# Optimization experiments

Hardware: AMD Instinct MI355X
Metric: run time of the kernel (lower is better)

The kernel has to match this reference:

```python
import jax, jax.numpy as jnp
import numpy as np

INPUT_SIZE = 512
HIDDEN_SIZE = 512
BATCH = 64
SEQ_LEN = 512


def _xavier(key, shape):
    fan_in, fan_out = shape[0], shape[1]
    limit = float(np.sqrt(6.0 / (fan_in + fan_out)))
    return jax.random.uniform(key, shape, jnp.float32, -limit, limit)


def setup_inputs() -> dict:
    key = jax.random.key(0)
    ks = jax.random.split(key, 14)
    inp = {
        "inputs": jax.random.normal(ks[0], (BATCH, SEQ_LEN, INPUT_SIZE), jnp.float32),
        "W_i": _xavier(ks[1], (INPUT_SIZE, HIDDEN_SIZE)),
        "W_f": _xavier(ks[2], (INPUT_SIZE, HIDDEN_SIZE)),
        "W_o": _xavier(ks[3], (INPUT_SIZE, HIDDEN_SIZE)),
        "W_c": _xavier(ks[4], (INPUT_SIZE, HIDDEN_SIZE)),
        "U_i": _xavier(ks[5], (HIDDEN_SIZE, HIDDEN_SIZE)),
        "U_f": _xavier(ks[6], (HIDDEN_SIZE, HIDDEN_SIZE)),
        "U_o": _xavier(ks[7], (HIDDEN_SIZE, HIDDEN_SIZE)),
        "U_c": _xavier(ks[8], (HIDDEN_SIZE, HIDDEN_SIZE)),
        "b_i": _xavier(ks[9], (1, HIDDEN_SIZE)),
        "b_f": _xavier(ks[10], (1, HIDDEN_SIZE)),
        "b_o": _xavier(ks[11], (1, HIDDEN_SIZE)),
        "b_c": _xavier(ks[12], (1, HIDDEN_SIZE)),
    }
    return inp


def reference(inputs, W_i, W_f, W_o, W_c, U_i, U_f, U_o, U_c, b_i, b_f, b_o, b_c):
    B, S, D = inputs.shape
    H = W_i.shape[1]
    # Fuse the 4 input projections into one GEMM over the whole sequence
    # (same math as per-step separate matmuls, just batched).
    W = jnp.concatenate([W_i, W_f, W_o, W_c], axis=1)      # [D, 4H]
    U = jnp.concatenate([U_i, U_f, U_o, U_c], axis=1)      # [H, 4H]
    b = jnp.concatenate([b_i, b_f, b_o, b_c], axis=1)      # [1, 4H]
    x_proj = jnp.einsum('bsd,dg->sbg', inputs, W) + b      # [S, B, 4H]

    def step(carry, xp):
        h, c = carry
        gates = xp + h @ U                                  # [B, 4H]
        i_g = jax.nn.sigmoid(gates[:, 0*H:1*H])
        f_g = jax.nn.sigmoid(gates[:, 1*H:2*H])
        o_g = jax.nn.sigmoid(gates[:, 2*H:3*H])
        c_t = jnp.tanh(gates[:, 3*H:4*H])
        c_new = f_g * c + i_g * c_t
        h_new = o_g * jnp.tanh(c_new)
        return (h_new, c_new), None

    h0 = jnp.zeros((B, H), jnp.float32)
    c0 = jnp.zeros((B, H), jnp.float32)
    (h_final, _), _ = jax.lax.scan(step, (h0, c0), x_proj)
    return h_final
```

## Files before the change

### kernel.cpp

```cpp
#include <hip/hip_runtime.h>


#define NGROUP 4
#define NSLICE 32
#define GROWS  16
#define SCOLS  16
#define DIM    512
#define HID    512
#define SEQ    512
#define NTHR   256
#define NWG    (NGROUP*NSLICE)

#define AOFF 0
#define BOFF 16384
#define LDS_BYTES (BOFF + 64*2048)

#define WS_CNT_BYTES 1024
#define HBUF_ELEMS   (2*NGROUP*GROWS*HID)
#define WS_NEED      (WS_CNT_BYTES + HBUF_ELEMS*2)

typedef float f32x4  __attribute__((ext_vector_type(4)));
typedef short bf16x8 __attribute__((ext_vector_type(8)));

__device__ __forceinline__ unsigned short f2bf(float f){
  union { float f; unsigned u; } v; v.f = f;
  unsigned r = v.u + 0x7fffu + ((v.u >> 16) & 1u);
  return (unsigned short)(r >> 16);
}
__device__ __forceinline__ float sigm(float x){ return 1.0f/(1.0f + __expf(-x)); }
__device__ __forceinline__ float tanh_f(float x){
  float e = __expf(-2.0f * fabsf(x));
  float t = (1.0f - e)/(1.0f + e);
  return x < 0.0f ? -t : t;
}

__global__ void zero_ws_kernel(uint4* p, int n4){
  int i = blockIdx.x*blockDim.x + threadIdx.x;
  uint4 z; z.x=0u; z.y=0u; z.z=0u; z.w=0u;
  if (i < n4) p[i] = z;
}

__global__ __launch_bounds__(NTHR, 1) void lstm_persistent(
  const float* __restrict__ x,
  const float* __restrict__ W0, const float* __restrict__ W1,
  const float* __restrict__ W2, const float* __restrict__ W3,
  const float* __restrict__ U0, const float* __restrict__ U1,
  const float* __restrict__ U2, const float* __restrict__ U3,
  const float* __restrict__ b0, const float* __restrict__ b1,
  const float* __restrict__ b2, const float* __restrict__ b3,
  float* __restrict__ out,
  unsigned* __restrict__ cnt,
  unsigned short* __restrict__ hbuf)
{
  __shared__ __align__(16) char smem[LDS_BYTES];
  const int tid = threadIdx.x;
  const int bid = blockIdx.x;
  const int g = bid >> 5;
  const int s = bid & 31;
  const int w = tid >> 6;
  const int l = tid & 63;

  {
    const int c    = tid & 63;
    const int kq   = tid >> 6;
    const int gate = c >> 4;
    const int cc   = c & 15;
    const int col  = s*SCOLS + cc;
    const float* Wsrc = (gate==0)?W0:(gate==1)?W1:(gate==2)?W2:W3;
    const float* Usrc = (gate==0)?U0:(gate==1)?U1:(gate==2)?U2:U3;
    const unsigned swz = (unsigned)((c & 7) << 4);
    char* Bp = &smem[BOFF + c*2048];
    #pragma unroll 4
    for (int k = kq*256; k < kq*256 + 256; ++k){
      float v = (k < DIM) ? Wsrc[(size_t)k*HID + col]
                          : Usrc[(size_t)(k-DIM)*HID + col];
      *(unsigned short*)(Bp + (((unsigned)(k*2)) ^ swz)) = f2bf(v);
    }
  }

  const int er = tid >> 4;
  const int ec = tid & 15;
  const int ecol = s*SCOLS + ec;
  const float bi = b0[ecol], bff = b1[ecol], bo = b2[ecol], bc = b3[ecol];
  float cstate = 0.0f;
  float hout   = 0.0f;

  const int arow = l & 15;
  const int qh   = l >> 4;
  const unsigned swzA = (unsigned)((arow & 7) << 4);
  const int bcol = w*16 + arow;
  const unsigned swzB = (unsigned)((bcol & 7) << 4);
  const char* Abase = &smem[AOFF + arow*1024];
  const char* Bbase = &smem[BOFF + bcol*2048];
  float* gatesLds = (float*)&smem[AOFF];

  const int sr  = tid >> 4;
  const int sdb = tid & 15;
  const unsigned swzS = (unsigned)((sr & 7) << 4);
  char* Arow = &smem[AOFF + sr*1024];

  unsigned* mycnt = &cnt[g*32];

  __syncthreads();

#define GEMM_STEP(QA, QB, ACC) do { \
    bf16x8 a_ = *(const bf16x8*)(Abase + (((unsigned)((QA)*64 + qh*16)) ^ swzA)); \
    bf16x8 b_ = *(const bf16x8*)(Bbase + (((unsigned)((QB)*64 + qh*16)) ^ swzB)); \
    ACC = __builtin_amdgcn_mfma_f32_16x16x32_bf16(a_, b_, ACC, 0, 0, 0); \
  } while(0)

  for (int t = 0; t < SEQ; ++t){
    {
      const float* xp = x + ((size_t)(g*GROWS + sr)*SEQ + (size_t)t)*DIM + sdb*32;
      #pragma unroll
      for (int j = 0; j < 4; ++j){
        f32x4 u = *(const f32x4*)(xp + j*8);
        f32x4 v = *(const f32x4*)(xp + j*8 + 4);
        bf16x8 o8;
        o8[0]=(short)f2bf(u[0]); o8[1]=(short)f2bf(u[1]);
        o8[2]=(short)f2bf(u[2]); o8[3]=(short)f2bf(u[3]);
        o8[4]=(short)f2bf(v[0]); o8[5]=(short)f2bf(v[1]);
        o8[6]=(short)f2bf(v[2]); o8[7]=(short)f2bf(v[3]);
        *(bf16x8*)(Arow + (((unsigned)(sdb*64 + j*16)) ^ swzS)) = o8;
      }
    }
    __syncthreads();

    f32x4 acc0 = {0.f,0.f,0.f,0.f}, acc1 = {0.f,0.f,0.f,0.f};
    f32x4 acc2 = {0.f,0.f,0.f,0.f}, acc3 = {0.f,0.f,0.f,0.f};

    #pragma unroll
    for (int q4 = 0; q4 < 4; ++q4){
      GEMM_STEP(q4*4+0, q4*4+0, acc0);
      GEMM_STEP(q4*4+1, q4*4+1, acc1);
      GEMM_STEP(q4*4+2, q4*4+2, acc2);
      GEMM_STEP(q4*4+3, q4*4+3, acc3);
    }

    if (t > 0 && tid == 0){
      const unsigned target = (unsigned)(32*t);
      while (__hip_atomic_load(mycnt, __ATOMIC_ACQUIRE, __HIP_MEMORY_SCOPE_AGENT) < target)
        __builtin_amdgcn_s_sleep(1);
    }
    __syncthreads();

    {
      const unsigned short* hsrc =
        hbuf + ((size_t)((t&1)*NGROUP + g)*GROWS + sr)*HID + sdb*32;
      #pragma unroll
      for (int j = 0; j < 4; ++j){
        bf16x8 hv = *(const bf16x8*)(hsrc + j*8);
        *(bf16x8*)(Arow + (((unsigned)(sdb*64 + j*16)) ^ swzS)) = hv;
      }
    }
    __syncthreads();

    #pragma unroll
    for (int q4 = 0; q4 < 4; ++q4){
      GEMM_STEP(q4*4+0, q4*4+16, acc0);
      GEMM_STEP(q4*4+1, q4*4+17, acc1);
      GEMM_STEP(q4*4+2, q4*4+18, acc2);
      GEMM_STEP(q4*4+3, q4*4+19, acc3);
    }
    __syncthreads();

    f32x4 accs = (acc0 + acc1) + (acc2 + acc3);
    #pragma unroll
    for (int rr = 0; rr < 4; ++rr)
      gatesLds[(qh*4 + rr)*64 + w*16 + arow] = accs[rr];
    __syncthreads();

    {
      float gi = gatesLds[er*64 +  0 + ec] + bi;
      float gf = gatesLds[er*64 + 16 + ec] + bff;
      float go = gatesLds[er*64 + 32 + ec] + bo;
      float gc = gatesLds[er*64 + 48 + ec] + bc;
      float ig = sigm(gi), fg = sigm(gf), og = sigm(go), ct = tanh_f(gc);
      cstate = fg*cstate + ig*ct;
      hout = og * tanh_f(cstate);
      hbuf[((size_t)(((t+1)&1)*NGROUP + g)*GROWS + er)*HID + s*SCOLS + ec] = f2bf(hout);
    }
    __syncthreads();

    if (tid == 0)
      __hip_atomic_fetch_add(mycnt, 1u, __ATOMIC_RELEASE, __HIP_MEMORY_SCOPE_AGENT);
  }

  out[(size_t)(g*GROWS + er)*HID + s*SCOLS + ec] = hout;
#undef GEMM_STEP
}

extern "C" void kernel_launch(void* const* d_in, const int* in_sizes, int n_in,
                              void* d_out, int out_size, void* d_ws, size_t ws_size,
                              hipStream_t stream)
{
  (void)in_sizes; (void)n_in; (void)out_size;
  if (ws_size < (size_t)WS_NEED) return;

  const float* x  = (const float*)d_in[0];
  const float* W0 = (const float*)d_in[1];
  const float* W1 = (const float*)d_in[2];
  const float* W2 = (const float*)d_in[3];
  const float* W3 = (const float*)d_in[4];
  const float* U0 = (const float*)d_in[5];
  const float* U1 = (const float*)d_in[6];
  const float* U2 = (const float*)d_in[7];
  const float* U3 = (const float*)d_in[8];
  const float* b0 = (const float*)d_in[9];
  const float* b1 = (const float*)d_in[10];
  const float* b2 = (const float*)d_in[11];
  const float* b3 = (const float*)d_in[12];
  float* out = (float*)d_out;

  unsigned* cnt = (unsigned*)d_ws;
  unsigned short* hbuf = (unsigned short*)((char*)d_ws + WS_CNT_BYTES);

  const int n4 = WS_NEED / 16;
  zero_ws_kernel<<<dim3((n4 + 255)/256), dim3(256), 0, stream>>>((uint4*)d_ws, n4);
  lstm_persistent<<<dim3(NWG), dim3(NTHR), 0, stream>>>(
      x, W0,W1,W2,W3, U0,U1,U2,U3, b0,b1,b2,b3, out, cnt, hbuf);
}
```

Before: 2.918 ms.

## Split batch into 8 groups of 8 rows across 256 workgroups

Doubles the workgroup count by partitioning the batch into 8 groups of 8 rows instead of 4 groups of 16. The MFMA A tile duplicates rows 0-7 and only half of the outputs are written, so each step does half the x/h loading and element-wise work per workgroup. Weight staging now uses vectorized float4 loads, and the block-to-group mapping is interleaved. The cost is that half the MFMA throughput is wasted on duplicate rows, and more workgroups join the per-group barrier.

```diff
diff --git a/kernel.cpp b/kernel.cpp
--- a/kernel.cpp
+++ b/kernel.cpp
@@ -1,22 +1,22 @@
 #include <hip/hip_runtime.h>
 
 
-#define NGROUP 4
-#define NSLICE 32
-#define GROWS  16
-#define SCOLS  16
-#define DIM    512
-#define HID    512
-#define SEQ    512
-#define NTHR   256
-#define NWG    (NGROUP*NSLICE)
+#define NG   8
+#define GR   8
+#define NS   32
+#define SC   16
+#define DIM  512
+#define HID  512
+#define SEQ  512
+#define NTHR 256
+#define NWG  (NG*NS)
 
 #define AOFF 0
-#define BOFF 16384
+#define BOFF (GR*1024)
 #define LDS_BYTES (BOFF + 64*2048)
 
 #define WS_CNT_BYTES 1024
-#define HBUF_ELEMS   (2*NGROUP*GROWS*HID)
+#define HBUF_ELEMS   (2*NG*GR*HID)
 #define WS_NEED      (WS_CNT_BYTES + HBUF_ELEMS*2)
 
 typedef float f32x4  __attribute__((ext_vector_type(4)));
@@ -55,47 +55,53 @@
   __shared__ __align__(16) char smem[LDS_BYTES];
   const int tid = threadIdx.x;
   const int bid = blockIdx.x;
-  const int g = bid >> 5;
-  const int s = bid & 31;
+  const int g = bid & 7;
+  const int s = bid >> 3;
   const int w = tid >> 6;
   const int l = tid & 63;
 
   {
-    const int c    = tid & 63;
-    const int kq   = tid >> 6;
-    const int gate = c >> 4;
-    const int cc   = c & 15;
-    const int col  = s*SCOLS + cc;
-    const float* Wsrc = (gate==0)?W0:(gate==1)?W1:(gate==2)?W2:W3;
-    const float* Usrc = (gate==0)?U0:(gate==1)?U1:(gate==2)?U2:U3;
-    const unsigned swz = (unsigned)((c & 7) << 4);
-    char* Bp = &smem[BOFF + c*2048];
-    #pragma unroll 4
-    for (int k = kq*256; k < kq*256 + 256; ++k){
-      float v = (k < DIM) ? Wsrc[(size_t)k*HID + col]
-                          : Usrc[(size_t)(k-DIM)*HID + col];
-      *(unsigned short*)(Bp + (((unsigned)(k*2)) ^ swz)) = f2bf(v);
+    const int q  = tid & 3;
+    const int kk = tid >> 2;
+    for (int gate = 0; gate < 4; ++gate){
+      const float* Wsrc = (gate==0)?W0:(gate==1)?W1:(gate==2)?W2:W3;
+      const float* Usrc = (gate==0)?U0:(gate==1)?U1:(gate==2)?U2:U3;
+      #pragma unroll
+      for (int kb = 0; kb < 16; ++kb){
+        const int k = kb*64 + kk;
+        const float* p = (k < DIM)
+          ? (Wsrc + (size_t)k*HID + s*SC + q*4)
+          : (Usrc + (size_t)(k-DIM)*HID + s*SC + q*4);
+        f32x4 v = *(const f32x4*)p;
+        #pragma unroll
+        for (int j = 0; j < 4; ++j){
+          const int c = gate*16 + q*4 + j;
+          const unsigned byte = ((unsigned)(k*2)) ^ ((unsigned)((c&7)<<4));
+          *(unsigned short*)(&smem[BOFF + c*2048] + byte) = f2bf(v[j]);
+        }
+      }
     }
   }
 
   const int er = tid >> 4;
   const int ec = tid & 15;
-  const int ecol = s*SCOLS + ec;
-  const float bi = b0[ecol], bff = b1[ecol], bo = b2[ecol], bc = b3[ecol];
-  float cstate = 0.0f;
-  float hout   = 0.0f;
+  const int ecol = s*SC + ec;
+  const bool ew = (tid < 128);
+  const float bi  = ew ? b0[ecol] : 0.f;
+  const float bff = ew ? b1[ecol] : 0.f;
+  const float bo  = ew ? b2[ecol] : 0.f;
+  const float bc  = ew ? b3[ecol] : 0.f;
+  float cstate = 0.0f, hout = 0.0f;
 
   const int arow = l & 15;
   const int qh   = l >> 4;
-  const unsigned swzA = (unsigned)((arow & 7) << 4);
-  const int bcol = w*16 + arow;
-  const unsigned swzB = (unsigned)((bcol & 7) << 4);
-  const char* Abase = &smem[AOFF + arow*1024];
-  const char* Bbase = &smem[BOFF + bcol*2048];
+  const unsigned swz = (unsigned)((arow & 7) << 4);
+  const char* Abase = &smem[AOFF + (arow & 7)*1024];
+  const char* Bbase = &smem[BOFF + (w*16 + arow)*2048];
   float* gatesLds = (float*)&smem[AOFF];
 
-  const int sr  = tid >> 4;
-  const int sdb = tid & 15;
+  const int sr   = tid >> 5;
+  const int sc16 = tid & 31;
   const unsigned swzS = (unsigned)((sr & 7) << 4);
   char* Arow = &smem[AOFF + sr*1024];
 
@@ -104,25 +110,29 @@
   __syncthreads();
 
 #define GEMM_STEP(QA, QB, ACC) do { \
-    bf16x8 a_ = *(const bf16x8*)(Abase + (((unsigned)((QA)*64 + qh*16)) ^ swzA)); \
-    bf16x8 b_ = *(const bf16x8*)(Bbase + (((unsigned)((QB)*64 + qh*16)) ^ swzB)); \
+    bf16x8 a_ = *(const bf16x8*)(Abase + (((unsigned)((QA)*64 + qh*16)) ^ swz)); \
+    bf16x8 b_ = *(const bf16x8*)(Bbase + (((unsigned)((QB)*64 + qh*16)) ^ swz)); \
     ACC = __builtin_amdgcn_mfma_f32_16x16x32_bf16(a_, b_, ACC, 0, 0, 0); \
   } while(0)
 
   for (int t = 0; t < SEQ; ++t){
     {
-      const float* xp = x + ((size_t)(g*GROWS + sr)*SEQ + (size_t)t)*DIM + sdb*32;
-      #pragma unroll
-      for (int j = 0; j < 4; ++j){
-        f32x4 u = *(const f32x4*)(xp + j*8);
-        f32x4 v = *(const f32x4*)(xp + j*8 + 4);
-        bf16x8 o8;
-        o8[0]=(short)f2bf(u[0]); o8[1]=(short)f2bf(u[1]);
-        o8[2]=(short)f2bf(u[2]); o8[3]=(short)f2bf(u[3]);
-        o8[4]=(short)f2bf(v[0]); o8[5]=(short)f2bf(v[1]);
-        o8[6]=(short)f2bf(v[2]); o8[7]=(short)f2bf(v[3]);
-        *(bf16x8*)(Arow + (((unsigned)(sdb*64 + j*16)) ^ swzS)) = o8;
-      }
+      const float* xp = x + ((size_t)(g*GR + sr)*SEQ + (size_t)t)*DIM + sc16*16;
+      f32x4 u0 = *(const f32x4*)(xp + 0);
+      f32x4 u1 = *(const f32x4*)(xp + 4);
+      f32x4 u2 = *(const f32x4*)(xp + 8);
+      f32x4 u3 = *(const f32x4*)(xp + 12);
+      bf16x8 o0, o1;
+      o0[0]=(short)f2bf(u0[0]); o0[1]=(short)f2bf(u0[1]);
+      o0[2]=(short)f2bf(u0[2]); o0[3]=(short)f2bf(u0[3]);
+      o0[4]=(short)f2bf(u1[0]); o0[5]=(short)f2bf(u1[1]);
+      o0[6]=(short)f2bf(u1[2]); o0[7]=(short)f2bf(u1[3]);
+      o1[0]=(short)f2bf(u2[0]); o1[1]=(short)f2bf(u2[1]);
+      o1[2]=(short)f2bf(u2[2]); o1[3]=(short)f2bf(u2[3]);
+      o1[4]=(short)f2bf(u3[0]); o1[5]=(short)f2bf(u3[1]);
+      o1[6]=(short)f2bf(u3[2]); o1[7]=(short)f2bf(u3[3]);
+      *(bf16x8*)(Arow + (((unsigned)(sc16*32 +  0)) ^ swzS)) = o0;
+      *(bf16x8*)(Arow + (((unsigned)(sc16*32 + 16)) ^ swzS)) = o1;
     }
     __syncthreads();
 
@@ -146,12 +156,11 @@
 
     {
       const unsigned short* hsrc =
-        hbuf + ((size_t)((t&1)*NGROUP + g)*GROWS + sr)*HID + sdb*32;
-      #pragma unroll
-      for (int j = 0; j < 4; ++j){
-        bf16x8 hv = *(const bf16x8*)(hsrc + j*8);
-        *(bf16x8*)(Arow + (((unsigned)(sdb*64 + j*16)) ^ swzS)) = hv;
-      }
+        hbuf + ((size_t)((t&1)*NG + g)*GR + sr)*HID + sc16*16;
+      bf16x8 h0 = *(const bf16x8*)(hsrc + 0);
+      bf16x8 h1 = *(const bf16x8*)(hsrc + 8);
+      *(bf16x8*)(Arow + (((unsigned)(sc16*32 +  0)) ^ swzS)) = h0;
+      *(bf16x8*)(Arow + (((unsigned)(sc16*32 + 16)) ^ swzS)) = h1;
     }
     __syncthreads();
 
@@ -165,12 +174,14 @@
     __syncthreads();
 
     f32x4 accs = (acc0 + acc1) + (acc2 + acc3);
-    #pragma unroll
-    for (int rr = 0; rr < 4; ++rr)
-      gatesLds[(qh*4 + rr)*64 + w*16 + arow] = accs[rr];
-    __syncthreads();
-
-    {
+    if (qh < 2){
+      #pragma unroll
+      for (int rr = 0; rr < 4; ++rr)
+        gatesLds[(qh*4 + rr)*64 + w*16 + arow] = accs[rr];
+    }
+    __syncthreads();
+
+    if (ew){
       float gi = gatesLds[er*64 +  0 + ec] + bi;
       float gf = gatesLds[er*64 + 16 + ec] + bff;
       float go = gatesLds[er*64 + 32 + ec] + bo;
@@ -178,7 +189,7 @@
       float ig = sigm(gi), fg = sigm(gf), og = sigm(go), ct = tanh_f(gc);
       cstate = fg*cstate + ig*ct;
       hout = og * tanh_f(cstate);
-      hbuf[((size_t)(((t+1)&1)*NGROUP + g)*GROWS + er)*HID + s*SCOLS + ec] = f2bf(hout);
+      hbuf[((size_t)(((t+1)&1)*NG + g)*GR + er)*HID + s*SC + ec] = f2bf(hout);
     }
     __syncthreads();
 
@@ -186,7 +197,8 @@
       __hip_atomic_fetch_add(mycnt, 1u, __ATOMIC_RELEASE, __HIP_MEMORY_SCOPE_AGENT);
   }
 
-  out[(size_t)(g*GROWS + er)*HID + s*SCOLS + ec] = hout;
+  if (ew)
+    out[(size_t)(g*GR + er)*HID + s*SC + ec] = hout;
 #undef GEMM_STEP
 }
 
```

Measured after the change: 4.245 ms. +45.5%, slower.
